# Kernel tuning notes

Measured on AMD Instinct MI355X. Metric: run time of the kernel, lower is better.

## Reference

```python
import jax, jax.numpy as jnp
import numpy as np

ALPHA = 1.0


def setup_inputs() -> dict:
    key = jax.random.key(0)
    ks = jax.random.split(key, 7)
    B, S, D_IN, D_OUT, R = 4, 2048, 2048, 2048, 64
    return {
        "x": jax.random.normal(ks[0], (B, S, D_IN), dtype=jnp.float32),
        "weight": jax.random.normal(ks[1], (D_OUT, D_IN), dtype=jnp.float32) * 0.02,
        "bias": jax.random.normal(ks[2], (D_OUT,), dtype=jnp.float32) * 0.02,
        "U": jax.random.normal(ks[3], (D_OUT, R), dtype=jnp.float32) * 0.02,
        "sigma": jax.random.normal(ks[4], (R, R), dtype=jnp.float32) * 0.02,
        "R": jax.random.normal(ks[5], (R, R), dtype=jnp.float32) * 0.02,
        "Vt": jax.random.normal(ks[6], (R, D_IN), dtype=jnp.float32) * 0.02,
    }


def reference(x, weight, bias, U, sigma, R, Vt):
    # base linear: F.linear(x, W, b) = x @ W^T + b
    base_out = jnp.einsum("bsi,oi->bso", x, weight) + bias
    # LoRA-XS delta: alpha * U @ sigma @ R @ Vt  -> [d_out, d_in]
    delta_W = ALPHA * (U @ sigma @ R @ Vt)
    lora_out = jnp.einsum("bsi,oi->bso", x, delta_W)
    return base_out + lora_out
```

## Files before the change

### kernel.cpp

```cpp
#include <hip/hip_runtime.h>
#include <hip/hip_bf16.h>
#include <stdint.h>

#define M_DIM 8192
#define K_DIM 2048
#define N_DIM 2048
#define RANK  64
#define ALPHA_F 1.0f

typedef __attribute__((ext_vector_type(4))) float  f32x4;
typedef __attribute__((ext_vector_type(8))) short  s16x8;

__device__ __forceinline__ unsigned short f2bf(float f) {
    unsigned int u = __float_as_uint(f);
    u += 0x7fffu + ((u >> 16) & 1u);
    return (unsigned short)(u >> 16);
}

__device__ __forceinline__ void gload_lds16(const void* g, void* l) {
    __builtin_amdgcn_global_load_lds(
        (const __attribute__((address_space(1))) void*)g,
        (__attribute__((address_space(3))) void*)l, 16, 0, 0);
}


__global__ __launch_bounds__(256) void t2sr_kernel(const float* __restrict__ sigma,
                                                   const float* __restrict__ Rm,
                                                   const float* __restrict__ Vt,
                                                   float* __restrict__ T2) {
    __shared__ float sSig[64];
    __shared__ float sRow[64];
    const int r = blockIdx.x >> 3;
    const int i = (blockIdx.x & 7) * 256 + threadIdx.x;
    if (threadIdx.x < 64) sSig[threadIdx.x] = sigma[r * 64 + threadIdx.x];
    __syncthreads();
    if (threadIdx.x < 64) {
        float a = 0.f;
        #pragma unroll 8
        for (int k = 0; k < 64; ++k) a += sSig[k] * Rm[k * 64 + threadIdx.x];
        sRow[threadIdx.x] = a;
    }
    __syncthreads();
    float a = 0.f;
    #pragma unroll 8
    for (int k = 0; k < 64; ++k) a += sRow[k] * Vt[k * 2048 + i];
    T2[r * 2048 + i] = a;
}

__global__ __launch_bounds__(256) void weffcast_kernel(const float* __restrict__ W,
                                                       const float* __restrict__ U,
                                                       const float* __restrict__ T2,
                                                       unsigned short* __restrict__ Wb,
                                                       const float* __restrict__ x,
                                                       unsigned short* __restrict__ xb) {
    __shared__ float sU[64 * 65];
    __shared__ float sT[64 * 64];
    if (blockIdx.x < 1024) {
        int to = blockIdx.x >> 5;
        int ti = blockIdx.x & 31;
        int o0 = to * 64, i0 = ti * 64;
        for (int e = 0; e < 16; ++e) {
            int li = threadIdx.x + e * 256;
            int hi = li >> 6, lo = li & 63;
            sU[hi * 65 + lo] = U[(size_t)o0 * 64 + li];
            sT[li]           = T2[hi * 2048 + i0 + lo];
        }
        __syncthreads();
        int o  = threadIdx.x >> 2;
        int ib = (threadIdx.x & 3) * 16;
        float acc[16] = {};
        for (int k = 0; k < 64; ++k) {
            float u = sU[o * 65 + k];
            #pragma unroll
            for (int j = 0; j < 16; ++j) acc[j] += u * sT[k * 64 + ib + j];
        }
        size_t base = (size_t)(o0 + o) * 2048 + i0 + ib;
        #pragma unroll
        for (int j = 0; j < 16; ++j)
            Wb[base + j] = f2bf(W[base + j] + ALPHA_F * acc[j]);
    } else {
        int cb = blockIdx.x - 1024;
        #pragma unroll
        for (int rep = 0; rep < 4; ++rep) {
            size_t idx = (((size_t)cb * 4 + rep) * 256 + threadIdx.x) * 8;
            f32x4 a = *reinterpret_cast<const f32x4*>(x + idx);
            f32x4 b = *reinterpret_cast<const f32x4*>(x + idx + 4);
            s16x8 o;
            o[0] = (short)f2bf(a[0]); o[1] = (short)f2bf(a[1]);
            o[2] = (short)f2bf(a[2]); o[3] = (short)f2bf(a[3]);
            o[4] = (short)f2bf(b[0]); o[5] = (short)f2bf(b[1]);
            o[6] = (short)f2bf(b[2]); o[7] = (short)f2bf(b[3]);
            *reinterpret_cast<s16x8*>(xb + idx) = o;
        }
    }
}


#define AHALF_E (128 * K_DIM)

__device__ __forceinline__ void stage_slot(const unsigned short* g0, const unsigned short* g1,
                                           char* smp, int ldsbase, int wave) {
    gload_lds16(g0, smp + ldsbase + wave * 1024);
    gload_lds16(g1, smp + ldsbase + 8192 + wave * 1024);
}

template <int B_, int P_>
__device__ __forceinline__ void read_frags(const char* sm, s16x8 (&af)[4],
                                           s16x8 (&bfr4)[4][2],
                                           int wr8, int wc4, int laneoff) {
    constexpr int ks = P_ & 1, mh = P_ >> 1;
    af[0] = *(const s16x8*)(sm + B_ * 32768 + ((wr8 + mh * 4 + 0) * 2 + ks) * 1024 + laneoff);
    if (P_ < 2) {
        #pragma unroll
        for (int ni = 0; ni < 4; ++ni)
            bfr4[ni][ks] = *(const s16x8*)(sm + 65536 + B_ * 32768 +
                              ((wc4 + ni) * 2 + ks) * 1024 + laneoff);
    }
    #pragma unroll
    for (int mi = 1; mi < 4; ++mi)
        af[mi] = *(const s16x8*)(sm + B_ * 32768 +
                    ((wr8 + mh * 4 + mi) * 2 + ks) * 1024 + laneoff);
}

template <int P_>
__device__ __forceinline__ void mfma_p(f32x4 (&acc)[8][4], s16x8 (&af)[4], s16x8 (&bfr4)[4][2]) {
    constexpr int ks = P_ & 1, mh = P_ >> 1;
    #pragma unroll
    for (int mi = 0; mi < 4; ++mi)
        #pragma unroll
        for (int ni = 0; ni < 4; ++ni)
            acc[mh * 4 + mi][ni] = __builtin_amdgcn_mfma_f32_16x16x32_bf16(
                af[mi], bfr4[ni][ks], acc[mh * 4 + mi][ni], 0, 0, 0);
}

#define VMWAIT2 do { asm volatile("s_waitcnt vmcnt(2)" ::: "memory"); \
                     __builtin_amdgcn_sched_barrier(0); } while (0)
#define VMWAIT4 do { asm volatile("s_waitcnt vmcnt(4)" ::: "memory"); \
                     __builtin_amdgcn_sched_barrier(0); } while (0)

#define DO_PHASE(B_, P_, STAGE_STMT, WAIT_STMT)                         \
  { s16x8 af[4];                                                        \
    read_frags<B_, P_>(sm, af, bfr4, wr8, wc4, laneoff);                \
    STAGE_STMT;                                                         \
    WAIT_STMT;                                                          \
    __builtin_amdgcn_s_barrier();                                       \
    __builtin_amdgcn_s_setprio(1);                                      \
    mfma_p<P_>(acc, af, bfr4);                                          \
    __builtin_amdgcn_s_setprio(0); }

#define STAGE_A(half, buf, kel) \
    stage_slot(Ag + (half) * AHALF_E + (kel) + soff0, Ag + (half) * AHALF_E + (kel) + soff1, \
               sm, (buf) * 32768 + (half) * 16384, wave)
#define STAGE_B(half, buf, kel) \
    stage_slot(Bg + (half) * AHALF_E + (kel) + soff0, Bg + (half) * AHALF_E + (kel) + soff1, \
               sm, 65536 + (buf) * 32768 + (half) * 16384, wave)

__global__ __launch_bounds__(512, 2)
void gemm8_kernel(const unsigned short* __restrict__ A,
                  const unsigned short* __restrict__ Bm,
                  const float* __restrict__ bias,
                  float* __restrict__ C) {
    extern __shared__ char sm[];

    const int tid  = threadIdx.x;
    const int wave = tid >> 6;
    const int lane = tid & 63;
    const int wr8  = (wave >> 2) * 8;
    const int wc4  = (wave & 3) * 4;

    const int bid = blockIdx.x;
    const int swz = (bid & 7) * 32 + (bid >> 3);
    const int rowM0 = (swz >> 3) * 256;
    const int rowN0 = (swz & 7) * 256;

    const unsigned short* Ag = A  + (size_t)rowM0 * K_DIM;
    const unsigned short* Bg = Bm + (size_t)rowN0 * K_DIM;

    int soff0, soff1;
    {
        #pragma unroll
        for (int ld = 0; ld < 2; ++ld) {
            int D   = ld * 8192 + tid * 16;
            int st  = D >> 10;
            int s   = (D >> 4) & 63;
            int row = s >> 2;
            int kq  = (s & 3) ^ ((s >> 3) & 3);
            int e = ((st >> 1) * 16 + row) * K_DIM + (st & 1) * 32 + kq * 8;
            if (ld == 0) soff0 = e; else soff1 = e;
        }
    }

    const int laneoff = ((lane & 15) * 4 + ((lane >> 4) ^ (((lane & 15) >> 1) & 3))) * 16;

    f32x4 acc[8][4] = {};
    s16x8 bfr4[4][2];

    STAGE_A(0, 0, 0);
    STAGE_A(1, 0, 0);
    STAGE_B(0, 0, 0);
    STAGE_B(1, 0, 0);
    STAGE_B(0, 1, 64);
    STAGE_B(1, 1, 64);
    VMWAIT4;
    __builtin_amdgcn_s_barrier();

    for (int i = 0; i < 16; ++i) {
        const int kA12 = (2 * i + 1) * 64;
        const int kN2  = ((2 * i + 2) & 31) * 64;
        const int kN3  = ((2 * i + 3) & 31) * 64;

        DO_PHASE(0, 0, STAGE_A(0, 1, kA12), ((void)0));
        DO_PHASE(0, 1, STAGE_A(1, 1, kA12), ((void)0));
        DO_PHASE(0, 2, ((void)0),           ((void)0));
        DO_PHASE(0, 3, STAGE_B(0, 0, kN2),  VMWAIT2);
        DO_PHASE(1, 0, STAGE_B(1, 0, kN2),  ((void)0));
        DO_PHASE(1, 1, STAGE_A(0, 0, kN2),  ((void)0));
        DO_PHASE(1, 2, STAGE_A(1, 0, kN2),  ((void)0));
        DO_PHASE(1, 3, (STAGE_B(0, 1, kN3), STAGE_B(1, 1, kN3)), VMWAIT4);
    }

    const int col0  = rowN0 + (wc4 >> 2) * 64 + (lane & 15);
    const int row0w = rowM0 + (wr8 >> 3) * 128 + (lane >> 4) * 4;
    float bv[4];
    #pragma unroll
    for (int ni = 0; ni < 4; ++ni) bv[ni] = bias[col0 + ni * 16];
    #pragma unroll
    for (int mi = 0; mi < 8; ++mi)
        #pragma unroll
        for (int ni = 0; ni < 4; ++ni)
            #pragma unroll
            for (int r = 0; r < 4; ++r)
                C[(size_t)(row0w + mi * 16 + r) * N_DIM + col0 + ni * 16] =
                    acc[mi][ni][r] + bv[ni];
}


__global__ __launch_bounds__(256) void xt_kernel(const float* __restrict__ x,
                                                 const float* __restrict__ T2,
                                                 float* __restrict__ xt) {
    int idx = blockIdx.x * 256 + threadIdx.x;
    int m = idx >> 6, r = idx & 63;
    float acc = 0.f;
    for (int i = 0; i < K_DIM; ++i) acc += x[(size_t)m * K_DIM + i] * T2[r * K_DIM + i];
    xt[idx] = acc;
}

__global__ __launch_bounds__(256) void fgemm_kernel(const float* __restrict__ A,
                                                    const float* __restrict__ W,
                                                    const float* __restrict__ xt,
                                                    const float* __restrict__ U,
                                                    const float* __restrict__ bias,
                                                    float* __restrict__ C) {
    __shared__ float sA[64][17];
    __shared__ float sW[64][17];
    int bm = blockIdx.x >> 5;
    int bn = blockIdx.x & 31;
    int m0 = bm * 64, n0 = bn * 64;
    int tid = threadIdx.x;
    int tm = tid >> 4, tn = tid & 15;
    float acc[4][4] = {};
    for (int k0 = 0; k0 < K_DIM; k0 += 16) {
        int lr = tid >> 2;
        int lc = (tid & 3) * 4;
        #pragma unroll
        for (int j = 0; j < 4; ++j) {
            sA[lr][lc + j] = A[(size_t)(m0 + lr) * K_DIM + k0 + lc + j];
            sW[lr][lc + j] = W[(size_t)(n0 + lr) * K_DIM + k0 + lc + j];
        }
        __syncthreads();
        #pragma unroll
        for (int kk = 0; kk < 16; ++kk) {
            float av[4], wv[4];
            #pragma unroll
            for (int i = 0; i < 4; ++i) av[i] = sA[tm * 4 + i][kk];
            #pragma unroll
            for (int j = 0; j < 4; ++j) wv[j] = sW[tn * 4 + j][kk];
            #pragma unroll
            for (int i = 0; i < 4; ++i)
                #pragma unroll
                for (int j = 0; j < 4; ++j) acc[i][j] += av[i] * wv[j];
        }
        __syncthreads();
    }
    #pragma unroll
    for (int i = 0; i < 4; ++i) {
        int m = m0 + tm * 4 + i;
        #pragma unroll
        for (int j = 0; j < 4; ++j) {
            int n = n0 + tn * 4 + j;
            float l = 0.f;
            for (int r = 0; r < RANK; ++r) l += xt[(size_t)m * RANK + r] * U[(size_t)n * RANK + r];
            C[(size_t)m * N_DIM + n] = acc[i][j] + l + bias[n];
        }
    }
}

extern "C" void kernel_launch(void* const* d_in, const int* in_sizes, int n_in,
                              void* d_out, int out_size, void* d_ws, size_t ws_size,
                              hipStream_t stream) {
    const float* x      = (const float*)d_in[0];
    const float* weight = (const float*)d_in[1];
    const float* bias   = (const float*)d_in[2];
    const float* U      = (const float*)d_in[3];
    const float* sigma  = (const float*)d_in[4];
    const float* Rm     = (const float*)d_in[5];
    const float* Vt     = (const float*)d_in[6];
    float* out = (float*)d_out;
    char* ws = (char*)d_ws;

    const size_t XB_BYTES = (size_t)M_DIM * K_DIM * 2;
    const size_t WB_BYTES = (size_t)N_DIM * K_DIM * 2;
    const size_t T2_BYTES = (size_t)RANK * K_DIM * 4;
    const size_t MAIN_NEED = XB_BYTES + WB_BYTES + T2_BYTES;

    if (ws_size >= MAIN_NEED) {
        unsigned short* xb = (unsigned short*)ws;
        unsigned short* wb = (unsigned short*)(ws + XB_BYTES);
        float* T2 = (float*)(ws + XB_BYTES + WB_BYTES);

        hipFuncSetAttribute((const void*)gemm8_kernel,
                            hipFuncAttributeMaxDynamicSharedMemorySize, 131072);

        t2sr_kernel<<<512, 256, 0, stream>>>(sigma, Rm, Vt, T2);
        weffcast_kernel<<<3072, 256, 0, stream>>>(weight, U, T2, wb, x, xb);
        gemm8_kernel<<<(M_DIM / 256) * (N_DIM / 256), 512, 131072, stream>>>(xb, wb, bias, out);
    } else {
        float* T2 = (float*)ws;
        float* xt = (float*)(ws + T2_BYTES);
        t2sr_kernel<<<512, 256, 0, stream>>>(sigma, Rm, Vt, T2);
        xt_kernel<<<(M_DIM * RANK) / 256, 256, 0, stream>>>(x, T2, xt);
        fgemm_kernel<<<(M_DIM / 64) * (N_DIM / 64), 256, 0, stream>>>(x, weight, xt, U, bias, out);
    }
}
```

Measured before the change: 94.23 us.

## Fuse fp32-to-bf16 cast of x into GEMM A-tile staging

Drops the separate x cast pass and its bf16 workspace buffer. The GEMM now loads fp32 x tiles into registers, converts them to bf16 and writes them into LDS, interleaved with the existing phased MFMA pipeline. This removes a full write and reread of the casted activation, but doubles the global A-side bytes per tile and adds conversion VALU work and LDS waits inside the main loop.

```diff
diff --git a/kernel.cpp b/kernel.cpp
--- a/kernel.cpp
+++ b/kernel.cpp
@@ -47,52 +47,34 @@
     T2[r * 2048 + i] = a;
 }
 
-__global__ __launch_bounds__(256) void weffcast_kernel(const float* __restrict__ W,
-                                                       const float* __restrict__ U,
-                                                       const float* __restrict__ T2,
-                                                       unsigned short* __restrict__ Wb,
-                                                       const float* __restrict__ x,
-                                                       unsigned short* __restrict__ xb) {
+__global__ __launch_bounds__(256) void weff_kernel(const float* __restrict__ W,
+                                                   const float* __restrict__ U,
+                                                   const float* __restrict__ T2,
+                                                   unsigned short* __restrict__ Wb) {
     __shared__ float sU[64 * 65];
     __shared__ float sT[64 * 64];
-    if (blockIdx.x < 1024) {
-        int to = blockIdx.x >> 5;
-        int ti = blockIdx.x & 31;
-        int o0 = to * 64, i0 = ti * 64;
-        for (int e = 0; e < 16; ++e) {
-            int li = threadIdx.x + e * 256;
-            int hi = li >> 6, lo = li & 63;
-            sU[hi * 65 + lo] = U[(size_t)o0 * 64 + li];
-            sT[li]           = T2[hi * 2048 + i0 + lo];
-        }
-        __syncthreads();
-        int o  = threadIdx.x >> 2;
-        int ib = (threadIdx.x & 3) * 16;
-        float acc[16] = {};
-        for (int k = 0; k < 64; ++k) {
-            float u = sU[o * 65 + k];
-            #pragma unroll
-            for (int j = 0; j < 16; ++j) acc[j] += u * sT[k * 64 + ib + j];
-        }
-        size_t base = (size_t)(o0 + o) * 2048 + i0 + ib;
-        #pragma unroll
-        for (int j = 0; j < 16; ++j)
-            Wb[base + j] = f2bf(W[base + j] + ALPHA_F * acc[j]);
-    } else {
-        int cb = blockIdx.x - 1024;
-        #pragma unroll
-        for (int rep = 0; rep < 4; ++rep) {
-            size_t idx = (((size_t)cb * 4 + rep) * 256 + threadIdx.x) * 8;
-            f32x4 a = *reinterpret_cast<const f32x4*>(x + idx);
-            f32x4 b = *reinterpret_cast<const f32x4*>(x + idx + 4);
-            s16x8 o;
-            o[0] = (short)f2bf(a[0]); o[1] = (short)f2bf(a[1]);
-            o[2] = (short)f2bf(a[2]); o[3] = (short)f2bf(a[3]);
-            o[4] = (short)f2bf(b[0]); o[5] = (short)f2bf(b[1]);
-            o[6] = (short)f2bf(b[2]); o[7] = (short)f2bf(b[3]);
-            *reinterpret_cast<s16x8*>(xb + idx) = o;
-        }
-    }
+    int to = blockIdx.x >> 5;
+    int ti = blockIdx.x & 31;
+    int o0 = to * 64, i0 = ti * 64;
+    for (int e = 0; e < 16; ++e) {
+        int li = threadIdx.x + e * 256;
+        int hi = li >> 6, lo = li & 63;
+        sU[hi * 65 + lo] = U[(size_t)o0 * 64 + li];
+        sT[li]           = T2[hi * 2048 + i0 + lo];
+    }
+    __syncthreads();
+    int o  = threadIdx.x >> 2;
+    int ib = (threadIdx.x & 3) * 16;
+    float acc[16] = {};
+    for (int k = 0; k < 64; ++k) {
+        float u = sU[o * 65 + k];
+        #pragma unroll
+        for (int j = 0; j < 16; ++j) acc[j] += u * sT[k * 64 + ib + j];
+    }
+    size_t base = (size_t)(o0 + o) * 2048 + i0 + ib;
+    #pragma unroll
+    for (int j = 0; j < 16; ++j)
+        Wb[base + j] = f2bf(W[base + j] + ALPHA_F * acc[j]);
 }
 
 
@@ -102,6 +84,27 @@
                                            char* smp, int ldsbase, int wave) {
     gload_lds16(g0, smp + ldsbase + wave * 1024);
     gload_lds16(g1, smp + ldsbase + 8192 + wave * 1024);
+}
+
+__device__ __forceinline__ void loadA16(const float* g0, const float* g1, f32x4 (&r)[4]) {
+    r[0] = *(const f32x4*)(g0);
+    r[1] = *(const f32x4*)(g0 + 4);
+    r[2] = *(const f32x4*)(g1);
+    r[3] = *(const f32x4*)(g1 + 4);
+}
+
+__device__ __forceinline__ s16x8 cvt8(f32x4 a, f32x4 b) {
+    s16x8 o;
+    o[0] = (short)f2bf(a[0]); o[1] = (short)f2bf(a[1]);
+    o[2] = (short)f2bf(a[2]); o[3] = (short)f2bf(a[3]);
+    o[4] = (short)f2bf(b[0]); o[5] = (short)f2bf(b[1]);
+    o[6] = (short)f2bf(b[2]); o[7] = (short)f2bf(b[3]);
+    return o;
+}
+
+__device__ __forceinline__ void writeA16(char* sm, int ldsbase, int tid, f32x4 (&r)[4]) {
+    *(s16x8*)(sm + ldsbase + tid * 16)        = cvt8(r[0], r[1]);
+    *(s16x8*)(sm + ldsbase + 8192 + tid * 16) = cvt8(r[2], r[3]);
 }
 
 template <int B_, int P_>
@@ -137,26 +140,30 @@
                      __builtin_amdgcn_sched_barrier(0); } while (0)
 #define VMWAIT4 do { asm volatile("s_waitcnt vmcnt(4)" ::: "memory"); \
                      __builtin_amdgcn_sched_barrier(0); } while (0)
-
-#define DO_PHASE(B_, P_, STAGE_STMT, WAIT_STMT)                         \
+#define VMWAIT8 do { asm volatile("s_waitcnt vmcnt(8)" ::: "memory"); \
+                     __builtin_amdgcn_sched_barrier(0); } while (0)
+#define LGKM0   do { asm volatile("s_waitcnt lgkmcnt(0)" ::: "memory"); } while (0)
+
+#define DO_PHASE(B_, P_, PRE_STMT, WAIT_STMT, POST_STMT)                \
   { s16x8 af[4];                                                        \
     read_frags<B_, P_>(sm, af, bfr4, wr8, wc4, laneoff);                \
-    STAGE_STMT;                                                         \
+    PRE_STMT;                                                           \
     WAIT_STMT;                                                          \
     __builtin_amdgcn_s_barrier();                                       \
     __builtin_amdgcn_s_setprio(1);                                      \
     mfma_p<P_>(acc, af, bfr4);                                          \
-    __builtin_amdgcn_s_setprio(0); }
-
-#define STAGE_A(half, buf, kel) \
-    stage_slot(Ag + (half) * AHALF_E + (kel) + soff0, Ag + (half) * AHALF_E + (kel) + soff1, \
-               sm, (buf) * 32768 + (half) * 16384, wave)
+    __builtin_amdgcn_s_setprio(0);                                      \
+    POST_STMT; }
+
 #define STAGE_B(half, buf, kel) \
     stage_slot(Bg + (half) * AHALF_E + (kel) + soff0, Bg + (half) * AHALF_E + (kel) + soff1, \
                sm, 65536 + (buf) * 32768 + (half) * 16384, wave)
+#define LOAD_A(half, kel, R) \
+    loadA16(Axf + (half) * AHALF_E + (kel) + soff0, Axf + (half) * AHALF_E + (kel) + soff1, R)
+#define WRITE_A(half, buf, R) writeA16(sm, (buf) * 32768 + (half) * 16384, tid, R)
 
 __global__ __launch_bounds__(512, 2)
-void gemm8_kernel(const unsigned short* __restrict__ A,
+void gemm8_kernel(const float* __restrict__ X,
                   const unsigned short* __restrict__ Bm,
                   const float* __restrict__ bias,
                   float* __restrict__ C) {
@@ -173,8 +180,8 @@
     const int rowM0 = (swz >> 3) * 256;
     const int rowN0 = (swz & 7) * 256;
 
-    const unsigned short* Ag = A  + (size_t)rowM0 * K_DIM;
-    const unsigned short* Bg = Bm + (size_t)rowN0 * K_DIM;
+    const float*          Axf = X  + (size_t)rowM0 * K_DIM;
+    const unsigned short* Bg  = Bm + (size_t)rowN0 * K_DIM;
 
     int soff0, soff1;
     {
@@ -194,14 +201,19 @@
 
     f32x4 acc[8][4] = {};
     s16x8 bfr4[4][2];
-
-    STAGE_A(0, 0, 0);
-    STAGE_A(1, 0, 0);
+    f32x4 rA0[4], rA1[4];
+
+    LOAD_A(0, 0, rA0);
+    LOAD_A(1, 0, rA1);
+    WRITE_A(0, 0, rA0);
+    WRITE_A(1, 0, rA1);
     STAGE_B(0, 0, 0);
     STAGE_B(1, 0, 0);
     STAGE_B(0, 1, 64);
     STAGE_B(1, 1, 64);
     VMWAIT4;
+    LGKM0;
+    LOAD_A(0, 64, rA0);
     __builtin_amdgcn_s_barrier();
 
     for (int i = 0; i < 16; ++i) {
@@ -209,14 +221,15 @@
         const int kN2  = ((2 * i + 2) & 31) * 64;
         const int kN3  = ((2 * i + 3) & 31) * 64;
 
-        DO_PHASE(0, 0, STAGE_A(0, 1, kA12), ((void)0));
-        DO_PHASE(0, 1, STAGE_A(1, 1, kA12), ((void)0));
-        DO_PHASE(0, 2, ((void)0),           ((void)0));
-        DO_PHASE(0, 3, STAGE_B(0, 0, kN2),  VMWAIT2);
-        DO_PHASE(1, 0, STAGE_B(1, 0, kN2),  ((void)0));
-        DO_PHASE(1, 1, STAGE_A(0, 0, kN2),  ((void)0));
-        DO_PHASE(1, 2, STAGE_A(1, 0, kN2),  ((void)0));
-        DO_PHASE(1, 3, (STAGE_B(0, 1, kN3), STAGE_B(1, 1, kN3)), VMWAIT4);
+        DO_PHASE(0, 0, (WRITE_A(0, 1, rA0), LOAD_A(1, kA12, rA1)), ((void)0), LGKM0);
+        DO_PHASE(0, 1, (WRITE_A(1, 1, rA1)),                        ((void)0), LGKM0);
+        DO_PHASE(0, 2, ((void)0),                                   ((void)0), ((void)0));
+        DO_PHASE(0, 3, (STAGE_B(0, 0, kN2)),                        VMWAIT2,   ((void)0));
+        DO_PHASE(1, 0, (STAGE_B(1, 0, kN2), LOAD_A(0, kN2, rA0)),   ((void)0), ((void)0));
+        DO_PHASE(1, 1, (WRITE_A(0, 0, rA0), LOAD_A(1, kN2, rA1)),   ((void)0), LGKM0);
+        DO_PHASE(1, 2, (WRITE_A(1, 0, rA1)),                        ((void)0),
+                 do { LGKM0; LOAD_A(0, kN3, rA0); } while (0));
+        DO_PHASE(1, 3, (STAGE_B(0, 1, kN3), STAGE_B(1, 1, kN3)),    VMWAIT8,   ((void)0));
     }
 
     const int col0  = rowN0 + (wc4 >> 2) * 64 + (lane & 15);
@@ -308,22 +321,20 @@
     float* out = (float*)d_out;
     char* ws = (char*)d_ws;
 
-    const size_t XB_BYTES = (size_t)M_DIM * K_DIM * 2;
     const size_t WB_BYTES = (size_t)N_DIM * K_DIM * 2;
     const size_t T2_BYTES = (size_t)RANK * K_DIM * 4;
-    const size_t MAIN_NEED = XB_BYTES + WB_BYTES + T2_BYTES;
+    const size_t MAIN_NEED = WB_BYTES + T2_BYTES;
 
     if (ws_size >= MAIN_NEED) {
-        unsigned short* xb = (unsigned short*)ws;
-        unsigned short* wb = (unsigned short*)(ws + XB_BYTES);
-        float* T2 = (float*)(ws + XB_BYTES + WB_BYTES);
+        unsigned short* wb = (unsigned short*)ws;
+        float* T2 = (float*)(ws + WB_BYTES);
 
         hipFuncSetAttribute((const void*)gemm8_kernel,
                             hipFuncAttributeMaxDynamicSharedMemorySize, 131072);
 
         t2sr_kernel<<<512, 256, 0, stream>>>(sigma, Rm, Vt, T2);
-        weffcast_kernel<<<3072, 256, 0, stream>>>(weight, U, T2, wb, x, xb);
-        gemm8_kernel<<<(M_DIM / 256) * (N_DIM / 256), 512, 131072, stream>>>(xb, wb, bias, out);
+        weff_kernel<<<(N_DIM / 64) * (K_DIM / 64), 256, 0, stream>>>(weight, U, T2, wb);
+        gemm8_kernel<<<(M_DIM / 256) * (N_DIM / 256), 512, 131072, stream>>>(x, wb, bias, out);
     } else {
         float* T2 = (float*)ws;
         float* xt = (float*)(ws + T2_BYTES);
```

Measured after the change: 130.2 us. +38.1%, slower.
